# Performance work log

Measured on AMD Instinct MI355X. Metric: run time of the kernel, lower is better.

Reference implementation:

```python
import jax, jax.numpy as jnp
import numpy as np

N_NODES = 100000
N_EDGES = 1600000
D_IN = 128
D_OUT = 128
EPS = 1e-9


def setup_inputs() -> dict:
    key = jax.random.key(0)
    ks = jax.random.split(key, 8)
    x = jax.random.normal(ks[0], (N_NODES, D_IN), dtype=jnp.float32)
    edge_row = jax.random.randint(ks[1], (N_EDGES,), 0, N_NODES, dtype=jnp.int32)
    edge_col = jax.random.randint(ks[2], (N_EDGES,), 0, N_NODES, dtype=jnp.int32)
    edge_val = jax.random.uniform(ks[3], (N_EDGES,), dtype=jnp.float32)
    W = jax.random.normal(ks[4], (D_OUT, D_IN), dtype=jnp.float32) * (1.0 / np.sqrt(D_IN))
    b = jax.random.normal(ks[5], (D_OUT,), dtype=jnp.float32) * 0.01
    scale = jnp.ones((D_OUT,), dtype=jnp.float32)
    offset = jnp.zeros((D_OUT,), dtype=jnp.float32)
    return {"x": x, "edge_row": edge_row, "edge_col": edge_col, "edge_val": edge_val,
            "W": W, "b": b, "scale": scale, "offset": offset}


def reference(x, edge_row, edge_col, edge_val, W, b, scale, offset):
    # spmm: feat[i] = sum_e val[e] * x[col[e]] for edges with row[e]==i
    msgs = edge_val[:, None] * x[edge_col]                      # [E, D_IN]
    feat = jax.ops.segment_sum(msgs, edge_row, num_segments=N_NODES)  # [N, D_IN]
    # linear + ELU
    out = jax.nn.elu(feat @ W.T + b)                            # [N, D_OUT]
    # per-row mean/var normalization (biased var), scale/offset
    mean = jnp.mean(out, axis=1, keepdims=True)
    var = jnp.var(out, axis=1, keepdims=True) + EPS
    return (out - mean) * scale * jax.lax.rsqrt(var) + offset
```

## Files before the change

### kernel.cpp

```cpp
#include <hip/hip_runtime.h>
#include <cstddef>

#define D 128
#define EPSV 1e-9f
#define NB 8
#define LDA 136
#define MAXBKT 2048
#define CAP 2048
#define RB 512
#define CAPE 1280
#define SG 128

typedef __attribute__((ext_vector_type(8))) short bf16x8;
typedef __attribute__((ext_vector_type(4))) float f32x4;

__device__ __forceinline__ float wred64(float v) {
    #pragma unroll
    for (int off = 32; off > 0; off >>= 1) v += __shfl_xor(v, off, 64);
    return v;
}

__device__ __forceinline__ ushort f2bf(float f) {
    uint u = __float_as_uint(f);
    return (ushort)((u + 0x7fffu + ((u >> 16) & 1u)) >> 16);
}

__device__ __forceinline__ float bflo(uint u) { return __uint_as_float(u << 16); }
__device__ __forceinline__ float bfhi(uint u) { return __uint_as_float(u & 0xffff0000u); }

__device__ __forceinline__ void node_epilogue(
    float a0, float a1, int node, int lane,
    const float* __restrict__ bias, const float* __restrict__ scale,
    const float* __restrict__ offset, float* __restrict__ out)
{
    const float2 bv = ((const float2*)bias)[lane];
    float e0 = a0 + bv.x, e1 = a1 + bv.y;
    e0 = e0 > 0.f ? e0 : expm1f(e0);
    e1 = e1 > 0.f ? e1 : expm1f(e1);
    const float s_  = wred64(e0 + e1);
    const float sq  = wred64(e0 * e0 + e1 * e1);
    const float mean = s_ * (1.0f / D);
    const float var  = sq * (1.0f / D) - mean * mean;
    const float rs   = rsqrtf(var + EPSV);
    const float2 sv = ((const float2*)scale)[lane];
    const float2 ov = ((const float2*)offset)[lane];
    ((float2*)(out + (size_t)node * D))[lane] =
        make_float2((e0 - mean) * sv.x * rs + ov.x,
                    (e1 - mean) * sv.y * rs + ov.y);
}

__global__ __launch_bounds__(256) void init_cursor(int* __restrict__ cursor, int nBkt)
{
    const int b = blockIdx.x * 256 + threadIdx.x;
    if (b < nBkt) cursor[b] = b * CAPE;
}

__global__ __launch_bounds__(256, 3) void fused_scatter_xw(
    const int* __restrict__ erow, const int* __restrict__ ecol,
    const float* __restrict__ eval_, int* __restrict__ cursor,
    int2* __restrict__ staged,
    const float* __restrict__ x, const float* __restrict__ W,
    ushort* __restrict__ y,
    int nE, int chunk, int nSc, int nN)
{
    __shared__ char smem[(64 + 128) * LDA * 2];

    const int tid = threadIdx.x;

    if ((int)blockIdx.x < nSc) {
        int* cnt   = (int*)smem;
        int* gbase = cnt + RB;
        const int cq = blockIdx.x & (SG - 1);
        const int rq = blockIdx.x >> 7;
        const int b0 = rq * RB;
        const int s = cq * chunk;
        const int e = min(s + chunk, nE);
        if (s >= nE) return;

        for (int b = tid; b < RB; b += 256) cnt[b] = 0;
        __syncthreads();

        const int n4 = (e - s) >> 2;
        const int4* er4 = (const int4*)(erow + s);
        for (int g = tid; g < n4; g += 256) {
            const int4 r4 = er4[g];
            int b;
            b = (r4.x >> 6) - b0; if ((unsigned)b < RB) atomicAdd(&cnt[b], 1);
            b = (r4.y >> 6) - b0; if ((unsigned)b < RB) atomicAdd(&cnt[b], 1);
            b = (r4.z >> 6) - b0; if ((unsigned)b < RB) atomicAdd(&cnt[b], 1);
            b = (r4.w >> 6) - b0; if ((unsigned)b < RB) atomicAdd(&cnt[b], 1);
        }
        for (int i = s + (n4 << 2) + tid; i < e; i += 256) {
            const int b = (erow[i] >> 6) - b0;
            if ((unsigned)b < RB) atomicAdd(&cnt[b], 1);
        }
        __syncthreads();
        for (int b = tid; b < RB; b += 256) {
            const int c = cnt[b];
            gbase[b] = c ? atomicAdd(&cursor[b0 + b], c) : 0;
            cnt[b] = 0;
        }
        __syncthreads();
        const int4*   ec4 = (const int4*)(ecol + s);
        const float4* ev4 = (const float4*)(eval_ + s);
        for (int g = tid; g < n4; g += 256) {
            const int4   r4 = er4[g];
            const int4   c4 = ec4[g];
            const float4 v4 = ev4[g];
            #define SCAT1(RX, CX, VX) { \
                const int b = ((RX) >> 6) - b0; \
                if ((unsigned)b < RB) { \
                    const int pos = gbase[b] + atomicAdd(&cnt[b], 1); \
                    if (pos < (b0 + b + 1) * CAPE) \
                        staged[pos] = make_int2((CX) | (((RX) & 63) << 20), \
                                                __float_as_int(VX)); \
                } }
            SCAT1(r4.x, c4.x, v4.x)
            SCAT1(r4.y, c4.y, v4.y)
            SCAT1(r4.z, c4.z, v4.z)
            SCAT1(r4.w, c4.w, v4.w)
        }
        for (int i = s + (n4 << 2) + tid; i < e; i += 256) {
            const int r = erow[i];
            SCAT1(r, ecol[i], eval_[i])
        }
        #undef SCAT1
        return;
    }

    ushort* lx = (ushort*)smem;
    ushort* lw = (ushort*)(smem + 64 * LDA * 2);
    const int nbase = ((int)blockIdx.x - nSc) * 64;

    for (int i = tid; i < (D * D) / 4; i += 256) {
        const float4 wv = ((const float4*)W)[i];
        const int o = i >> 5, k = (4 * i) & 127;
        ushort4 h4;
        h4.x = f2bf(wv.x); h4.y = f2bf(wv.y); h4.z = f2bf(wv.z); h4.w = f2bf(wv.w);
        *(ushort4*)&lw[o * LDA + k] = h4;
    }
    for (int i = tid; i < 64 * 32; i += 256) {
        const int r = i >> 5, c4 = i & 31;
        float4 v = make_float4(0.f, 0.f, 0.f, 0.f);
        if (nbase + r < nN) v = *(const float4*)&x[(size_t)(nbase + r) * D + c4 * 4];
        ushort4 h4;
        h4.x = f2bf(v.x); h4.y = f2bf(v.y); h4.z = f2bf(v.z); h4.w = f2bf(v.w);
        *(ushort4*)&lx[r * LDA + c4 * 4] = h4;
    }
    __syncthreads();

    const int w = tid >> 6, l = tid & 63;
    const int m = l & 15, g = l >> 4;
    const int rbase = w * 16;

    f32x4 acc[8] = {};
    #pragma unroll
    for (int kk = 0; kk < 4; ++kk) {
        const int k0 = kk * 32 + g * 8;
        const bf16x8 a = *(const bf16x8*)&lx[(rbase + m) * LDA + k0];
        #pragma unroll
        for (int t = 0; t < 8; ++t) {
            const bf16x8 b = *(const bf16x8*)&lw[(t * 16 + m) * LDA + k0];
            acc[t] = __builtin_amdgcn_mfma_f32_16x16x32_bf16(a, b, acc[t], 0, 0, 0);
        }
    }

    #pragma unroll
    for (int t = 0; t < 8; ++t) {
        #pragma unroll
        for (int r = 0; r < 4; ++r) {
            const int row = nbase + rbase + g * 4 + r;
            if (row < nN)
                y[(size_t)row * D + t * 16 + m] = f2bf(acc[t][r]);
        }
    }
}

__global__ __launch_bounds__(256) void bucket_spmm_epi(
    const ushort* __restrict__ y, const int* __restrict__ cursor,
    const int2* __restrict__ staged, const float* __restrict__ bias,
    const float* __restrict__ scale, const float* __restrict__ offset,
    float* __restrict__ out, int nN)
{
    __shared__ int2 ledge2[CAP];
    __shared__ int  lhist[64];
    __shared__ int  lfill[64];
    __shared__ int  lptr[65];

    const int tid  = threadIdx.x;
    const int lane = tid & 63;
    const int w    = tid >> 6;
    const int bkt  = blockIdx.x;
    const int s = bkt * CAPE;
    const int e = min(cursor[bkt], s + CAPE);
    const int cnt = e - s;
    const int nodeBase = bkt * 64;
    const char* yb = (const char*)y;
    const int lo4 = lane * 4;

    if (tid < 64) { lhist[tid] = 0; lfill[tid] = 0; }
    __syncthreads();
    for (int i = tid; i < cnt; i += 256)
        atomicAdd(&lhist[staged[s + i].x >> 20], 1);
    __syncthreads();
    if (w == 0) {
        int inc = lhist[lane];
        #pragma unroll
        for (int d = 1; d < 64; d <<= 1) {
            const int t = __shfl_up(inc, d, 64);
            if (lane >= d) inc += t;
        }
        lptr[lane + 1] = inc;
        if (lane == 0) lptr[0] = 0;
    }
    __syncthreads();
    for (int i = tid; i < cnt; i += 256) {
        const int2 ed = staged[s + i];
        const int r = ed.x >> 20;
        const int pos = lptr[r] + atomicAdd(&lfill[r], 1);
        ledge2[pos] = make_int2((ed.x & 0xFFFFF) << 8, ed.y);
    }
    __syncthreads();

    #pragma unroll
    for (int r16 = 0; r16 < 16; ++r16) {
        const int r = w * 16 + r16;
        const int node = nodeBase + r;
        if (node >= nN) break;
        const int js = lptr[r], je = lptr[r + 1];
        float a0 = 0.f, a1 = 0.f, b0 = 0.f, b1 = 0.f;
        int j = js;
        for (; j + 7 < je; j += 8) {
            const int2 e0 = ledge2[j],     e1 = ledge2[j + 1];
            const int2 e2 = ledge2[j + 2], e3 = ledge2[j + 3];
            const int2 e4 = ledge2[j + 4], e5 = ledge2[j + 5];
            const int2 e6 = ledge2[j + 6], e7 = ledge2[j + 7];
            const uint u0 = *(const uint*)(yb + e0.x + lo4);
            const uint u1 = *(const uint*)(yb + e1.x + lo4);
            const uint u2 = *(const uint*)(yb + e2.x + lo4);
            const uint u3 = *(const uint*)(yb + e3.x + lo4);
            const uint u4 = *(const uint*)(yb + e4.x + lo4);
            const uint u5 = *(const uint*)(yb + e5.x + lo4);
            const uint u6 = *(const uint*)(yb + e6.x + lo4);
            const uint u7 = *(const uint*)(yb + e7.x + lo4);
            const float v0 = __int_as_float(e0.y), v1 = __int_as_float(e1.y);
            const float v2 = __int_as_float(e2.y), v3 = __int_as_float(e3.y);
            const float v4 = __int_as_float(e4.y), v5 = __int_as_float(e5.y);
            const float v6 = __int_as_float(e6.y), v7 = __int_as_float(e7.y);
            a0 = fmaf(v0, bflo(u0), a0); a1 = fmaf(v0, bfhi(u0), a1);
            b0 = fmaf(v1, bflo(u1), b0); b1 = fmaf(v1, bfhi(u1), b1);
            a0 = fmaf(v2, bflo(u2), a0); a1 = fmaf(v2, bfhi(u2), a1);
            b0 = fmaf(v3, bflo(u3), b0); b1 = fmaf(v3, bfhi(u3), b1);
            a0 = fmaf(v4, bflo(u4), a0); a1 = fmaf(v4, bfhi(u4), a1);
            b0 = fmaf(v5, bflo(u5), b0); b1 = fmaf(v5, bfhi(u5), b1);
            a0 = fmaf(v6, bflo(u6), a0); a1 = fmaf(v6, bfhi(u6), a1);
            b0 = fmaf(v7, bflo(u7), b0); b1 = fmaf(v7, bfhi(u7), b1);
        }
        for (; j + 3 < je; j += 4) {
            const int2 e0 = ledge2[j],     e1 = ledge2[j + 1];
            const int2 e2 = ledge2[j + 2], e3 = ledge2[j + 3];
            const uint u0 = *(const uint*)(yb + e0.x + lo4);
            const uint u1 = *(const uint*)(yb + e1.x + lo4);
            const uint u2 = *(const uint*)(yb + e2.x + lo4);
            const uint u3 = *(const uint*)(yb + e3.x + lo4);
            const float v0 = __int_as_float(e0.y), v1 = __int_as_float(e1.y);
            const float v2 = __int_as_float(e2.y), v3 = __int_as_float(e3.y);
            a0 = fmaf(v0, bflo(u0), a0); a1 = fmaf(v0, bfhi(u0), a1);
            b0 = fmaf(v1, bflo(u1), b0); b1 = fmaf(v1, bfhi(u1), b1);
            a0 = fmaf(v2, bflo(u2), a0); a1 = fmaf(v2, bfhi(u2), a1);
            b0 = fmaf(v3, bflo(u3), b0); b1 = fmaf(v3, bfhi(u3), b1);
        }
        for (; j < je; ++j) {
            const int2 e0 = ledge2[j];
            const uint u0 = *(const uint*)(yb + e0.x + lo4);
            const float v0 = __int_as_float(e0.y);
            a0 = fmaf(v0, bflo(u0), a0); a1 = fmaf(v0, bfhi(u0), a1);
        }
        node_epilogue(a0 + b0, a1 + b1, node, lane, bias, scale, offset, out);
    }
}

__global__ __launch_bounds__(256) void spmm_atomic_kernel(
    const float* __restrict__ x, const int* __restrict__ erow,
    const int* __restrict__ ecol, const float* __restrict__ eval_,
    float* __restrict__ feat, int nEdges)
{
    const int lane = threadIdx.x & 63;
    int w = (int)((blockIdx.x * blockDim.x + threadIdx.x) >> 6);
    const int nW = (int)((gridDim.x * blockDim.x) >> 6);
    for (int e = w; e < nEdges; e += nW) {
        const int r = erow[e];
        const int c = ecol[e];
        const float v = eval_[e];
        const float2 xv = ((const float2*)(x + (size_t)c * D))[lane];
        float* fr = feat + (size_t)r * D + 2 * lane;
        unsafeAtomicAdd(fr,     v * xv.x);
        unsafeAtomicAdd(fr + 1, v * xv.y);
    }
}

#define LW(i) const float4 w##i = Wp[i];
#define LW_ALL  LW(0) LW(1) LW(2) LW(3) LW(4) LW(5) LW(6) LW(7) \
                LW(8) LW(9) LW(10) LW(11) LW(12) LW(13) LW(14) LW(15) \
                LW(16) LW(17) LW(18) LW(19) LW(20) LW(21) LW(22) LW(23) \
                LW(24) LW(25) LW(26) LW(27) LW(28) LW(29) LW(30) LW(31)
#define GST(i) { const float4 f = Lf[i]; \
    a0 = fmaf(f.x, w##i.x, a0); a1 = fmaf(f.y, w##i.y, a1); \
    a2 = fmaf(f.z, w##i.z, a2); a3 = fmaf(f.w, w##i.w, a3); }
#define GST_ALL GST(0) GST(1) GST(2) GST(3) GST(4) GST(5) GST(6) GST(7) \
                GST(8) GST(9) GST(10) GST(11) GST(12) GST(13) GST(14) GST(15) \
                GST(16) GST(17) GST(18) GST(19) GST(20) GST(21) GST(22) GST(23) \
                GST(24) GST(25) GST(26) GST(27) GST(28) GST(29) GST(30) GST(31)

__global__ __launch_bounds__(256, 2) void gemm_epi_f32(
    const float* in, float* outp,
    const float* __restrict__ W, const float* __restrict__ bias,
    const float* __restrict__ scale, const float* __restrict__ offset,
    int nNodes)
{
    __shared__ float  lfeat[NB][D];
    __shared__ float2 red[2][4][2];

    const int tid  = threadIdx.x;
    const int wave = tid >> 6;
    const int lane = tid & 63;
    const int p = wave >> 1;
    const int h = wave & 1;
    const int o = h * 64 + lane;

    const float4* Wp = (const float4*)(W + (size_t)o * D);
    LW_ALL
    const float bo = bias[o], sco = scale[o], ofo = offset[o];

    const int r_st = tid >> 5;
    const int q    = tid & 31;

    for (int nbase = blockIdx.x * NB; nbase < nNodes; nbase += gridDim.x * NB) {
        {
            const int node = nbase + r_st;
            float4 v = make_float4(0.f, 0.f, 0.f, 0.f);
            if (node < nNodes) v = *(const float4*)&in[(size_t)node * D + q * 4];
            *(float4*)&lfeat[r_st][q * 4] = v;
        }
        __syncthreads();
        float e[4];
        #pragma unroll
        for (int nd = 0; nd < 4; ++nd) {
            const float4* Lf = (const float4*)lfeat[p * 4 + nd];
            float a0 = 0.f, a1 = 0.f, a2 = 0.f, a3 = 0.f;
            GST_ALL
            float v = (a0 + a1) + (a2 + a3) + bo;
            v = v > 0.f ? v : expm1f(v);
            e[nd] = v;
            const float s  = wred64(v);
            const float sq = wred64(v * v);
            if (lane == 0) red[p][nd][h] = make_float2(s, sq);
        }
        __syncthreads();
        #pragma unroll
        for (int nd = 0; nd < 4; ++nd) {
            const int node = nbase + p * 4 + nd;
            if (node < nNodes) {
                const float2 r0 = red[p][nd][0];
                const float2 r1 = red[p][nd][1];
                const float s  = r0.x + r1.x;
                const float sq = r0.y + r1.y;
                const float mean = s * (1.0f / D);
                const float var  = sq * (1.0f / D) - mean * mean;
                const float rs   = rsqrtf(var + EPSV);
                outp[(size_t)node * D + o] = (e[nd] - mean) * sco * rs + ofo;
            }
        }
        __syncthreads();
    }
}

extern "C" void kernel_launch(void* const* d_in, const int* in_sizes, int n_in,
                              void* d_out, int out_size, void* d_ws, size_t ws_size,
                              hipStream_t stream) {
    const float* x      = (const float*)d_in[0];
    const int*   erow   = (const int*)d_in[1];
    const int*   ecol   = (const int*)d_in[2];
    const float* eval_  = (const float*)d_in[3];
    const float* W      = (const float*)d_in[4];
    const float* bias   = (const float*)d_in[5];
    const float* scale  = (const float*)d_in[6];
    const float* offset = (const float*)d_in[7];
    float* out = (float*)d_out;

    const int nE = in_sizes[1];
    const int nN = in_sizes[0] / D;
    const int nBkt = (nN + 63) >> 6;

    size_t off = 0;
    auto take = [&](size_t bytes) {
        size_t o = off;
        off = (off + bytes + 255) & ~(size_t)255;
        return o;
    };
    const size_t o_cursor = take((size_t)(MAXBKT + 4) * 4);
    const size_t o_staged = take((size_t)nBkt * CAPE * 8);
    const size_t o_y      = take((size_t)nN * D * 2);
    const size_t need = off;

    const bool fast = (ws_size >= need) && (nBkt <= MAXBKT) &&
                      ((size_t)nE <= (size_t)nBkt * (CAPE - 256) || nBkt == 0);

    if (fast) {
        char* ws = (char*)d_ws;
        int*  cursor = (int*)(ws + o_cursor);
        int2* staged = (int2*)(ws + o_staged);
        ushort* y    = (ushort*)(ws + o_y);

        init_cursor<<<(nBkt + 255) / 256, 256, 0, stream>>>(cursor, nBkt);

        const int chunk = (((nE + SG - 1) / SG) + 3) & ~3;
        const int nRange = (nBkt + RB - 1) / RB;
        const int nSc = SG * nRange;
        const int nXW = (nN + 63) / 64;
        fused_scatter_xw<<<nSc + nXW, 256, 0, stream>>>(
            erow, ecol, eval_, cursor, staged, x, W, y, nE, chunk, nSc, nN);

        bucket_spmm_epi<<<nBkt, 256, 0, stream>>>(
            y, cursor, staged, bias, scale, offset, out, nN);
    } else {
        hipMemsetAsync(out, 0, (size_t)nN * D * sizeof(float), stream);
        spmm_atomic_kernel<<<2048, 256, 0, stream>>>(x, erow, ecol, eval_, out, nE);
        gemm_epi_f32<<<(nN + NB - 1) / NB, 256, 0, stream>>>(
            out, out, W, bias, scale, offset, nN);
    }
}
```

Baseline: 113.0 us.

## Replace per-bucket edge sort with fixed-point LDS atomic accumulation; halve GEMM LDS

The bucket SpMM kernel no longer histograms and sorts edges by row into LDS. Each wave instead streams its share of staged edges and accumulates into a 64x128 integer LDS tile with fixed-point atomic adds. The edge encoding is reworked so the column is pre-shifted into a byte offset, which removes the local reordering pass and its extra staged reads. The x*W tile is loaded in two K-halves to shrink LDS and raise the occupancy hint from 3 to 5, and the int4-vectorised scatter loops are dropped for scalar loops. The fixed-point scale risks precision loss and integer overflow, and LDS atomic contention may be costly.

After: 179.7 us. +59.1%, slower.

```diff
diff --git a/kernel.cpp b/kernel.cpp
--- a/kernel.cpp
+++ b/kernel.cpp
@@ -4,12 +4,13 @@
 #define D 128
 #define EPSV 1e-9f
 #define NB 8
-#define LDA 136
+#define LDAH 72
 #define MAXBKT 2048
-#define CAP 2048
 #define RB 512
 #define CAPE 1280
 #define SG 128
+#define FXSCALE 2097152.0f
+#define FXINV   (1.0f / 2097152.0f)
 
 typedef __attribute__((ext_vector_type(8))) short bf16x8;
 typedef __attribute__((ext_vector_type(4))) float f32x4;
@@ -55,7 +56,7 @@
     if (b < nBkt) cursor[b] = b * CAPE;
 }
 
-__global__ __launch_bounds__(256, 3) void fused_scatter_xw(
+__global__ __launch_bounds__(256, 5) void fused_scatter_xw(
     const int* __restrict__ erow, const int* __restrict__ ecol,
     const float* __restrict__ eval_, int* __restrict__ cursor,
     int2* __restrict__ staged,
@@ -63,7 +64,7 @@
     ushort* __restrict__ y,
     int nE, int chunk, int nSc, int nN)
 {
-    __shared__ char smem[(64 + 128) * LDA * 2];
+    __shared__ char smem[(64 + 128) * LDAH * 2];
 
     const int tid = threadIdx.x;
 
@@ -79,18 +80,7 @@
 
         for (int b = tid; b < RB; b += 256) cnt[b] = 0;
         __syncthreads();
-
-        const int n4 = (e - s) >> 2;
-        const int4* er4 = (const int4*)(erow + s);
-        for (int g = tid; g < n4; g += 256) {
-            const int4 r4 = er4[g];
-            int b;
-            b = (r4.x >> 6) - b0; if ((unsigned)b < RB) atomicAdd(&cnt[b], 1);
-            b = (r4.y >> 6) - b0; if ((unsigned)b < RB) atomicAdd(&cnt[b], 1);
-            b = (r4.z >> 6) - b0; if ((unsigned)b < RB) atomicAdd(&cnt[b], 1);
-            b = (r4.w >> 6) - b0; if ((unsigned)b < RB) atomicAdd(&cnt[b], 1);
-        }
-        for (int i = s + (n4 << 2) + tid; i < e; i += 256) {
+        for (int i = s + tid; i < e; i += 256) {
             const int b = (erow[i] >> 6) - b0;
             if ((unsigned)b < RB) atomicAdd(&cnt[b], 1);
         }
@@ -101,53 +91,22 @@
             cnt[b] = 0;
         }
         __syncthreads();
-        const int4*   ec4 = (const int4*)(ecol + s);
-        const float4* ev4 = (const float4*)(eval_ + s);
-        for (int g = tid; g < n4; g += 256) {
-            const int4   r4 = er4[g];
-            const int4   c4 = ec4[g];
-            const float4 v4 = ev4[g];
-            #define SCAT1(RX, CX, VX) { \
-                const int b = ((RX) >> 6) - b0; \
-                if ((unsigned)b < RB) { \
-                    const int pos = gbase[b] + atomicAdd(&cnt[b], 1); \
-                    if (pos < (b0 + b + 1) * CAPE) \
-                        staged[pos] = make_int2((CX) | (((RX) & 63) << 20), \
-                                                __float_as_int(VX)); \
-                } }
-            SCAT1(r4.x, c4.x, v4.x)
-            SCAT1(r4.y, c4.y, v4.y)
-            SCAT1(r4.z, c4.z, v4.z)
-            SCAT1(r4.w, c4.w, v4.w)
-        }
-        for (int i = s + (n4 << 2) + tid; i < e; i += 256) {
+        for (int i = s + tid; i < e; i += 256) {
             const int r = erow[i];
-            SCAT1(r, ecol[i], eval_[i])
-        }
-        #undef SCAT1
+            const int b = (r >> 6) - b0;
+            if ((unsigned)b < RB) {
+                const int pos = gbase[b] + atomicAdd(&cnt[b], 1);
+                if (pos < (b0 + b + 1) * CAPE)
+                    staged[pos] = make_int2((ecol[i] << 8) | ((r & 63) << 26),
+                                            __float_as_int(eval_[i]));
+            }
+        }
         return;
     }
 
     ushort* lx = (ushort*)smem;
-    ushort* lw = (ushort*)(smem + 64 * LDA * 2);
+    ushort* lw = (ushort*)(smem + 64 * LDAH * 2);
     const int nbase = ((int)blockIdx.x - nSc) * 64;
-
-    for (int i = tid; i < (D * D) / 4; i += 256) {
-        const float4 wv = ((const float4*)W)[i];
-        const int o = i >> 5, k = (4 * i) & 127;
-        ushort4 h4;
-        h4.x = f2bf(wv.x); h4.y = f2bf(wv.y); h4.z = f2bf(wv.z); h4.w = f2bf(wv.w);
-        *(ushort4*)&lw[o * LDA + k] = h4;
-    }
-    for (int i = tid; i < 64 * 32; i += 256) {
-        const int r = i >> 5, c4 = i & 31;
-        float4 v = make_float4(0.f, 0.f, 0.f, 0.f);
-        if (nbase + r < nN) v = *(const float4*)&x[(size_t)(nbase + r) * D + c4 * 4];
-        ushort4 h4;
-        h4.x = f2bf(v.x); h4.y = f2bf(v.y); h4.z = f2bf(v.z); h4.w = f2bf(v.w);
-        *(ushort4*)&lx[r * LDA + c4 * 4] = h4;
-    }
-    __syncthreads();
 
     const int w = tid >> 6, l = tid & 63;
     const int m = l & 15, g = l >> 4;
@@ -155,13 +114,36 @@
 
     f32x4 acc[8] = {};
     #pragma unroll
-    for (int kk = 0; kk < 4; ++kk) {
-        const int k0 = kk * 32 + g * 8;
-        const bf16x8 a = *(const bf16x8*)&lx[(rbase + m) * LDA + k0];
+    for (int half = 0; half < 2; ++half) {
+        if (half) __syncthreads();
+        const int kbase = half * 64;
+        for (int i = tid; i < (D * 64) / 4; i += 256) {
+            const int o = i >> 4, k4 = i & 15;
+            const float4 wv = *(const float4*)&W[(size_t)o * D + kbase + k4 * 4];
+            ushort4 h4;
+            h4.x = f2bf(wv.x); h4.y = f2bf(wv.y); h4.z = f2bf(wv.z); h4.w = f2bf(wv.w);
+            *(ushort4*)&lw[o * LDAH + k4 * 4] = h4;
+        }
+        for (int i = tid; i < (64 * 64) / 4; i += 256) {
+            const int r = i >> 4, k4 = i & 15;
+            float4 v = make_float4(0.f, 0.f, 0.f, 0.f);
+            if (nbase + r < nN)
+                v = *(const float4*)&x[(size_t)(nbase + r) * D + kbase + k4 * 4];
+            ushort4 h4;
+            h4.x = f2bf(v.x); h4.y = f2bf(v.y); h4.z = f2bf(v.z); h4.w = f2bf(v.w);
+            *(ushort4*)&lx[r * LDAH + k4 * 4] = h4;
+        }
+        __syncthreads();
+
         #pragma unroll
-        for (int t = 0; t < 8; ++t) {
-            const bf16x8 b = *(const bf16x8*)&lw[(t * 16 + m) * LDA + k0];
-            acc[t] = __builtin_amdgcn_mfma_f32_16x16x32_bf16(a, b, acc[t], 0, 0, 0);
+        for (int kk = 0; kk < 2; ++kk) {
+            const int k0 = kk * 32 + g * 8;
+            const bf16x8 a = *(const bf16x8*)&lx[(rbase + m) * LDAH + k0];
+            #pragma unroll
+            for (int t = 0; t < 8; ++t) {
+                const bf16x8 b = *(const bf16x8*)&lw[(t * 16 + m) * LDAH + k0];
+                acc[t] = __builtin_amdgcn_mfma_f32_16x16x32_bf16(a, b, acc[t], 0, 0, 0);
+            }
         }
     }
 
@@ -182,10 +164,7 @@
     const float* __restrict__ scale, const float* __restrict__ offset,
     float* __restrict__ out, int nN)
 {
-    __shared__ int2 ledge2[CAP];
-    __shared__ int  lhist[64];
-    __shared__ int  lfill[64];
-    __shared__ int  lptr[65];
+    __shared__ int acc[64][D];
 
     const int tid  = threadIdx.x;
     const int lane = tid & 63;
@@ -198,85 +177,55 @@
     const char* yb = (const char*)y;
     const int lo4 = lane * 4;
 
-    if (tid < 64) { lhist[tid] = 0; lfill[tid] = 0; }
+    for (int i = tid; i < (64 * D) / 4; i += 256)
+        ((int4*)acc)[i] = make_int4(0, 0, 0, 0);
     __syncthreads();
-    for (int i = tid; i < cnt; i += 256)
-        atomicAdd(&lhist[staged[s + i].x >> 20], 1);
-    __syncthreads();
-    if (w == 0) {
-        int inc = lhist[lane];
-        #pragma unroll
-        for (int d = 1; d < 64; d <<= 1) {
-            const int t = __shfl_up(inc, d, 64);
-            if (lane >= d) inc += t;
-        }
-        lptr[lane + 1] = inc;
-        if (lane == 0) lptr[0] = 0;
-    }
-    __syncthreads();
-    for (int i = tid; i < cnt; i += 256) {
-        const int2 ed = staged[s + i];
-        const int r = ed.x >> 20;
-        const int pos = lptr[r] + atomicAdd(&lfill[r], 1);
-        ledge2[pos] = make_int2((ed.x & 0xFFFFF) << 8, ed.y);
+
+    const int q  = (cnt + 3) >> 2;
+    const int js = s + w * q;
+    const int je = min(js + q, e);
+
+    int j = js;
+    for (; j + 3 < je; j += 4) {
+        const int2 e0 = staged[j],     e1 = staged[j + 1];
+        const int2 e2 = staged[j + 2], e3 = staged[j + 3];
+        const uint u0 = *(const uint*)(yb + (e0.x & 0x03FFFF00) + lo4);
+        const uint u1 = *(const uint*)(yb + (e1.x & 0x03FFFF00) + lo4);
+        const uint u2 = *(const uint*)(yb + (e2.x & 0x03FFFF00) + lo4);
+        const uint u3 = *(const uint*)(yb + (e3.x & 0x03FFFF00) + lo4);
+        const float v0 = __int_as_float(e0.y) * FXSCALE;
+        const float v1 = __int_as_float(e1.y) * FXSCALE;
+        const float v2 = __int_as_float(e2.y) * FXSCALE;
+        const float v3 = __int_as_float(e3.y) * FXSCALE;
+        const int r0 = (uint)e0.x >> 26, r1 = (uint)e1.x >> 26;
+        const int r2 = (uint)e2.x >> 26, r3 = (uint)e3.x >> 26;
+        atomicAdd(&acc[r0][2 * lane],     (int)(v0 * bflo(u0)));
+        atomicAdd(&acc[r0][2 * lane + 1], (int)(v0 * bfhi(u0)));
+        atomicAdd(&acc[r1][2 * lane],     (int)(v1 * bflo(u1)));
+        atomicAdd(&acc[r1][2 * lane + 1], (int)(v1 * bfhi(u1)));
+        atomicAdd(&acc[r2][2 * lane],     (int)(v2 * bflo(u2)));
+        atomicAdd(&acc[r2][2 * lane + 1], (int)(v2 * bfhi(u2)));
+        atomicAdd(&acc[r3][2 * lane],     (int)(v3 * bflo(u3)));
+        atomicAdd(&acc[r3][2 * lane + 1], (int)(v3 * bfhi(u3)));
+    }
+    for (; j < je; ++j) {
+        const int2 e0 = staged[j];
+        const uint u0 = *(const uint*)(yb + (e0.x & 0x03FFFF00) + lo4);
+        const float v0 = __int_as_float(e0.y) * FXSCALE;
+        const int r0 = (uint)e0.x >> 26;
+        atomicAdd(&acc[r0][2 * lane],     (int)(v0 * bflo(u0)));
+        atomicAdd(&acc[r0][2 * lane + 1], (int)(v0 * bfhi(u0)));
     }
     __syncthreads();
 
     #pragma unroll
     for (int r16 = 0; r16 < 16; ++r16) {
-        const int r = w * 16 + r16;
-        const int node = nodeBase + r;
+        const int row  = w * 16 + r16;
+        const int node = nodeBase + row;
         if (node >= nN) break;
-        const int js = lptr[r], je = lptr[r + 1];
-        float a0 = 0.f, a1 = 0.f, b0 = 0.f, b1 = 0.f;
-        int j = js;
-        for (; j + 7 < je; j += 8) {
-            const int2 e0 = ledge2[j],     e1 = ledge2[j + 1];
-            const int2 e2 = ledge2[j + 2], e3 = ledge2[j + 3];
-            const int2 e4 = ledge2[j + 4], e5 = ledge2[j + 5];
-            const int2 e6 = ledge2[j + 6], e7 = ledge2[j + 7];
-            const uint u0 = *(const uint*)(yb + e0.x + lo4);
-            const uint u1 = *(const uint*)(yb + e1.x + lo4);
-            const uint u2 = *(const uint*)(yb + e2.x + lo4);
-            const uint u3 = *(const uint*)(yb + e3.x + lo4);
-            const uint u4 = *(const uint*)(yb + e4.x + lo4);
-            const uint u5 = *(const uint*)(yb + e5.x + lo4);
-            const uint u6 = *(const uint*)(yb + e6.x + lo4);
-            const uint u7 = *(const uint*)(yb + e7.x + lo4);
-            const float v0 = __int_as_float(e0.y), v1 = __int_as_float(e1.y);
-            const float v2 = __int_as_float(e2.y), v3 = __int_as_float(e3.y);
-            const float v4 = __int_as_float(e4.y), v5 = __int_as_float(e5.y);
-            const float v6 = __int_as_float(e6.y), v7 = __int_as_float(e7.y);
-            a0 = fmaf(v0, bflo(u0), a0); a1 = fmaf(v0, bfhi(u0), a1);
-            b0 = fmaf(v1, bflo(u1), b0); b1 = fmaf(v1, bfhi(u1), b1);
-            a0 = fmaf(v2, bflo(u2), a0); a1 = fmaf(v2, bfhi(u2), a1);
-            b0 = fmaf(v3, bflo(u3), b0); b1 = fmaf(v3, bfhi(u3), b1);
-            a0 = fmaf(v4, bflo(u4), a0); a1 = fmaf(v4, bfhi(u4), a1);
-            b0 = fmaf(v5, bflo(u5), b0); b1 = fmaf(v5, bfhi(u5), b1);
-            a0 = fmaf(v6, bflo(u6), a0); a1 = fmaf(v6, bfhi(u6), a1);
-            b0 = fmaf(v7, bflo(u7), b0); b1 = fmaf(v7, bfhi(u7), b1);
-        }
-        for (; j + 3 < je; j += 4) {
-            const int2 e0 = ledge2[j],     e1 = ledge2[j + 1];
-            const int2 e2 = ledge2[j + 2], e3 = ledge2[j + 3];
-            const uint u0 = *(const uint*)(yb + e0.x + lo4);
-            const uint u1 = *(const uint*)(yb + e1.x + lo4);
-            const uint u2 = *(const uint*)(yb + e2.x + lo4);
-            const uint u3 = *(const uint*)(yb + e3.x + lo4);
-            const float v0 = __int_as_float(e0.y), v1 = __int_as_float(e1.y);
-            const float v2 = __int_as_float(e2.y), v3 = __int_as_float(e3.y);
-            a0 = fmaf(v0, bflo(u0), a0); a1 = fmaf(v0, bfhi(u0), a1);
-            b0 = fmaf(v1, bflo(u1), b0); b1 = fmaf(v1, bfhi(u1), b1);
-            a0 = fmaf(v2, bflo(u2), a0); a1 = fmaf(v2, bfhi(u2), a1);
-            b0 = fmaf(v3, bflo(u3), b0); b1 = fmaf(v3, bfhi(u3), b1);
-        }
-        for (; j < je; ++j) {
-            const int2 e0 = ledge2[j];
-            const uint u0 = *(const uint*)(yb + e0.x + lo4);
-            const float v0 = __int_as_float(e0.y);
-            a0 = fmaf(v0, bflo(u0), a0); a1 = fmaf(v0, bfhi(u0), a1);
-        }
-        node_epilogue(a0 + b0, a1 + b1, node, lane, bias, scale, offset, out);
+        const float a0 = (float)acc[row][2 * lane]     * FXINV;
+        const float a1 = (float)acc[row][2 * lane + 1] * FXINV;
+        node_epilogue(a0, a1, node, lane, bias, scale, offset, out);
     }
 }
 
@@ -414,7 +363,7 @@
 
         init_cursor<<<(nBkt + 255) / 256, 256, 0, stream>>>(cursor, nBkt);
 
-        const int chunk = (((nE + SG - 1) / SG) + 3) & ~3;
+        const int chunk = (nE + SG - 1) / SG;
         const int nRange = (nBkt + RB - 1) / RB;
         const int nSc = SG * nRange;
         const int nXW = (nN + 63) / 64;
```

## Halve LDS footprint, split GEMM K loop, widen SpMM blocks to 512 threads

Applied to the files above, without the earlier changes.

The x·W tile GEMM now stages W and x in two K-halves with a 72-element stride, halving shared memory so the fused scatter/GEMM kernel can target 5 blocks per SM instead of 3. The scatter drops int4 vectorized loads for scalar loops and pre-shifts the column index (<<8) into the staged word, which removes a shift in the SpMM kernel. The bucket SpMM kernel uses 512 threads with 8 rows per wave and a smaller LDS edge buffer, raising parallelism per bucket. The risks are an extra barrier and reload in the GEMM and less vectorized global loads in the scatter.

After: 135.9 us. 20.3% more time.

```diff
diff --git a/kernel.cpp b/kernel.cpp
--- a/kernel.cpp
+++ b/kernel.cpp
@@ -4,9 +4,8 @@
 #define D 128
 #define EPSV 1e-9f
 #define NB 8
-#define LDA 136
+#define LDAH 72
 #define MAXBKT 2048
-#define CAP 2048
 #define RB 512
 #define CAPE 1280
 #define SG 128
@@ -55,7 +54,7 @@
     if (b < nBkt) cursor[b] = b * CAPE;
 }
 
-__global__ __launch_bounds__(256, 3) void fused_scatter_xw(
+__global__ __launch_bounds__(256, 5) void fused_scatter_xw(
     const int* __restrict__ erow, const int* __restrict__ ecol,
     const float* __restrict__ eval_, int* __restrict__ cursor,
     int2* __restrict__ staged,
@@ -63,7 +62,7 @@
     ushort* __restrict__ y,
     int nE, int chunk, int nSc, int nN)
 {
-    __shared__ char smem[(64 + 128) * LDA * 2];
+    __shared__ char smem[(64 + 128) * LDAH * 2];
 
     const int tid = threadIdx.x;
 
@@ -79,18 +78,7 @@
 
         for (int b = tid; b < RB; b += 256) cnt[b] = 0;
         __syncthreads();
-
-        const int n4 = (e - s) >> 2;
-        const int4* er4 = (const int4*)(erow + s);
-        for (int g = tid; g < n4; g += 256) {
-            const int4 r4 = er4[g];
-            int b;
-            b = (r4.x >> 6) - b0; if ((unsigned)b < RB) atomicAdd(&cnt[b], 1);
-            b = (r4.y >> 6) - b0; if ((unsigned)b < RB) atomicAdd(&cnt[b], 1);
-            b = (r4.z >> 6) - b0; if ((unsigned)b < RB) atomicAdd(&cnt[b], 1);
-            b = (r4.w >> 6) - b0; if ((unsigned)b < RB) atomicAdd(&cnt[b], 1);
-        }
-        for (int i = s + (n4 << 2) + tid; i < e; i += 256) {
+        for (int i = s + tid; i < e; i += 256) {
             const int b = (erow[i] >> 6) - b0;
             if ((unsigned)b < RB) atomicAdd(&cnt[b], 1);
         }
@@ -101,53 +89,22 @@
             cnt[b] = 0;
         }
         __syncthreads();
-        const int4*   ec4 = (const int4*)(ecol + s);
-        const float4* ev4 = (const float4*)(eval_ + s);
-        for (int g = tid; g < n4; g += 256) {
-            const int4   r4 = er4[g];
-            const int4   c4 = ec4[g];
-            const float4 v4 = ev4[g];
-            #define SCAT1(RX, CX, VX) { \
-                const int b = ((RX) >> 6) - b0; \
-                if ((unsigned)b < RB) { \
-                    const int pos = gbase[b] + atomicAdd(&cnt[b], 1); \
-                    if (pos < (b0 + b + 1) * CAPE) \
-                        staged[pos] = make_int2((CX) | (((RX) & 63) << 20), \
-                                                __float_as_int(VX)); \
-                } }
-            SCAT1(r4.x, c4.x, v4.x)
-            SCAT1(r4.y, c4.y, v4.y)
-            SCAT1(r4.z, c4.z, v4.z)
-            SCAT1(r4.w, c4.w, v4.w)
-        }
-        for (int i = s + (n4 << 2) + tid; i < e; i += 256) {
+        for (int i = s + tid; i < e; i += 256) {
             const int r = erow[i];
-            SCAT1(r, ecol[i], eval_[i])
-        }
-        #undef SCAT1
+            const int b = (r >> 6) - b0;
+            if ((unsigned)b < RB) {
+                const int pos = gbase[b] + atomicAdd(&cnt[b], 1);
+                if (pos < (b0 + b + 1) * CAPE)
+                    staged[pos] = make_int2((ecol[i] << 8) | ((r & 63) << 26),
+                                            __float_as_int(eval_[i]));
+            }
+        }
         return;
     }
 
     ushort* lx = (ushort*)smem;
-    ushort* lw = (ushort*)(smem + 64 * LDA * 2);
+    ushort* lw = (ushort*)(smem + 64 * LDAH * 2);
     const int nbase = ((int)blockIdx.x - nSc) * 64;
-
-    for (int i = tid; i < (D * D) / 4; i += 256) {
-        const float4 wv = ((const float4*)W)[i];
-        const int o = i >> 5, k = (4 * i) & 127;
-        ushort4 h4;
-        h4.x = f2bf(wv.x); h4.y = f2bf(wv.y); h4.z = f2bf(wv.z); h4.w = f2bf(wv.w);
-        *(ushort4*)&lw[o * LDA + k] = h4;
-    }
-    for (int i = tid; i < 64 * 32; i += 256) {
-        const int r = i >> 5, c4 = i & 31;
-        float4 v = make_float4(0.f, 0.f, 0.f, 0.f);
-        if (nbase + r < nN) v = *(const float4*)&x[(size_t)(nbase + r) * D + c4 * 4];
-        ushort4 h4;
-        h4.x = f2bf(v.x); h4.y = f2bf(v.y); h4.z = f2bf(v.z); h4.w = f2bf(v.w);
-        *(ushort4*)&lx[r * LDA + c4 * 4] = h4;
-    }
-    __syncthreads();
 
     const int w = tid >> 6, l = tid & 63;
     const int m = l & 15, g = l >> 4;
@@ -155,13 +112,36 @@
 
     f32x4 acc[8] = {};
     #pragma unroll
-    for (int kk = 0; kk < 4; ++kk) {
-        const int k0 = kk * 32 + g * 8;
-        const bf16x8 a = *(const bf16x8*)&lx[(rbase + m) * LDA + k0];
+    for (int half = 0; half < 2; ++half) {
+        if (half) __syncthreads();
+        const int kbase = half * 64;
+        for (int i = tid; i < (D * 64) / 4; i += 256) {
+            const int o = i >> 4, k4 = i & 15;
+            const float4 wv = *(const float4*)&W[(size_t)o * D + kbase + k4 * 4];
+            ushort4 h4;
+            h4.x = f2bf(wv.x); h4.y = f2bf(wv.y); h4.z = f2bf(wv.z); h4.w = f2bf(wv.w);
+            *(ushort4*)&lw[o * LDAH + k4 * 4] = h4;
+        }
+        for (int i = tid; i < (64 * 64) / 4; i += 256) {
+            const int r = i >> 4, k4 = i & 15;
+            float4 v = make_float4(0.f, 0.f, 0.f, 0.f);
+            if (nbase + r < nN)
+                v = *(const float4*)&x[(size_t)(nbase + r) * D + kbase + k4 * 4];
+            ushort4 h4;
+            h4.x = f2bf(v.x); h4.y = f2bf(v.y); h4.z = f2bf(v.z); h4.w = f2bf(v.w);
+            *(ushort4*)&lx[r * LDAH + k4 * 4] = h4;
+        }
+        __syncthreads();
+
         #pragma unroll
-        for (int t = 0; t < 8; ++t) {
-            const bf16x8 b = *(const bf16x8*)&lw[(t * 16 + m) * LDA + k0];
-            acc[t] = __builtin_amdgcn_mfma_f32_16x16x32_bf16(a, b, acc[t], 0, 0, 0);
+        for (int kk = 0; kk < 2; ++kk) {
+            const int k0 = kk * 32 + g * 8;
+            const bf16x8 a = *(const bf16x8*)&lx[(rbase + m) * LDAH + k0];
+            #pragma unroll
+            for (int t = 0; t < 8; ++t) {
+                const bf16x8 b = *(const bf16x8*)&lw[(t * 16 + m) * LDAH + k0];
+                acc[t] = __builtin_amdgcn_mfma_f32_16x16x32_bf16(a, b, acc[t], 0, 0, 0);
+            }
         }
     }
 
@@ -176,13 +156,13 @@
     }
 }
 
-__global__ __launch_bounds__(256) void bucket_spmm_epi(
+__global__ __launch_bounds__(512) void bucket_spmm_epi(
     const ushort* __restrict__ y, const int* __restrict__ cursor,
     const int2* __restrict__ staged, const float* __restrict__ bias,
     const float* __restrict__ scale, const float* __restrict__ offset,
     float* __restrict__ out, int nN)
 {
-    __shared__ int2 ledge2[CAP];
+    __shared__ int2 ledge2[CAPE];
     __shared__ int  lhist[64];
     __shared__ int  lfill[64];
     __shared__ int  lptr[65];
@@ -200,8 +180,8 @@
 
     if (tid < 64) { lhist[tid] = 0; lfill[tid] = 0; }
     __syncthreads();
-    for (int i = tid; i < cnt; i += 256)
-        atomicAdd(&lhist[staged[s + i].x >> 20], 1);
+    for (int i = tid; i < cnt; i += 512)
+        atomicAdd(&lhist[(uint)staged[s + i].x >> 26], 1);
     __syncthreads();
     if (w == 0) {
         int inc = lhist[lane];
@@ -214,17 +194,17 @@
         if (lane == 0) lptr[0] = 0;
     }
     __syncthreads();
-    for (int i = tid; i < cnt; i += 256) {
+    for (int i = tid; i < cnt; i += 512) {
         const int2 ed = staged[s + i];
-        const int r = ed.x >> 20;
+        const int r = (uint)ed.x >> 26;
         const int pos = lptr[r] + atomicAdd(&lfill[r], 1);
-        ledge2[pos] = make_int2((ed.x & 0xFFFFF) << 8, ed.y);
+        ledge2[pos] = make_int2(ed.x & 0x03FFFF00, ed.y);
     }
     __syncthreads();
 
     #pragma unroll
-    for (int r16 = 0; r16 < 16; ++r16) {
-        const int r = w * 16 + r16;
+    for (int r8 = 0; r8 < 8; ++r8) {
+        const int r = w * 8 + r8;
         const int node = nodeBase + r;
         if (node >= nN) break;
         const int js = lptr[r], je = lptr[r + 1];
@@ -414,14 +394,14 @@
 
         init_cursor<<<(nBkt + 255) / 256, 256, 0, stream>>>(cursor, nBkt);
 
-        const int chunk = (((nE + SG - 1) / SG) + 3) & ~3;
+        const int chunk = (nE + SG - 1) / SG;
         const int nRange = (nBkt + RB - 1) / RB;
         const int nSc = SG * nRange;
         const int nXW = (nN + 63) / 64;
         fused_scatter_xw<<<nSc + nXW, 256, 0, stream>>>(
             erow, ecol, eval_, cursor, staged, x, W, y, nE, chunk, nSc, nN);
 
-        bucket_spmm_epi<<<nBkt, 256, 0, stream>>>(
+        bucket_spmm_epi<<<nBkt, 512, 0, stream>>>(
             y, cursor, staged, bias, scale, offset, out, nN);
     } else {
         hipMemsetAsync(out, 0, (size_t)nN * D * sizeof(float), stream);
```
